# Kernel tuning notes

Hardware: AMD Instinct MI355X
Metric: run time of the kernel (lower is better)

## Reference

```python
import jax, jax.numpy as jnp
import numpy as np

B, T, D, H = 4, 2048, 1024, 16
HD = D // H  # 64
LOCAL_CTX, BLOCKSIZE, VERTSIZE = 256, 1, 16
STRIDE = LOCAL_CTX // BLOCKSIZE  # 256


def build_fixed_mask(n):
    # num_verts == 1 branch of generate_fixed_attention_mask
    layout = np.zeros((n, n), dtype=np.bool_)
    # vertical stripes: top `vertsize` indices of each stride block
    for idx in range(STRIDE - VERTSIZE, STRIDE):
        layout[:, idx::STRIDE] = True
    rows = np.arange(n)
    # local: each query attends to its own stride-block
    same_block = (rows[:, None] // STRIDE) == (rows[None, :] // STRIDE)
    layout |= same_block
    # causal: zero out k > q
    layout &= rows[None, :] <= rows[:, None]
    return layout


def setup_inputs() -> dict:
    key = jax.random.key(0)
    k1, k2, k3, k4, k5 = jax.random.split(key, 5)
    s = 0.02
    return {
        "x": jax.random.normal(k1, (B, T, D), dtype=jnp.float32),
        "Wqkv": jax.random.normal(k2, (D, 3 * D), dtype=jnp.float32) * s,
        "bqkv": jax.random.normal(k3, (3 * D,), dtype=jnp.float32) * s,
        "Wproj": jax.random.normal(k4, (D, D), dtype=jnp.float32) * s,
        "bproj": jax.random.normal(k5, (D,), dtype=jnp.float32) * s,
        "mask": jnp.asarray(build_fixed_mask(T)),
    }


def reference(x, Wqkv, bqkv, Wproj, bproj, mask):
    b, t, _ = x.shape
    qkv = (x @ Wqkv + bqkv).reshape(b, t, 3, H, HD)
    # (B,T,3,H,HD) -> (B,H,T,HD) per component
    q = qkv[:, :, 0].transpose(0, 2, 1, 3)
    k = qkv[:, :, 1].transpose(0, 2, 1, 3)
    v = qkv[:, :, 2].transpose(0, 2, 1, 3)
    att = jnp.einsum("bhqd,bhkd->bhqk", q, k) * (1.0 / jnp.sqrt(jnp.float32(HD)))
    att = jnp.where(mask[:t, :t], att, -jnp.inf)
    att = jax.nn.softmax(att, axis=-1)
    y = jnp.einsum("bhqk,bhkd->bhqd", att, v)
    y = y.transpose(0, 2, 1, 3).reshape(b, t, D)
    return y @ Wproj + bproj
```

## Files before the change

kernel.cpp:

```cpp
#include <hip/hip_runtime.h>
#include <cstdint>
#include <cstddef>

typedef unsigned short u16;
typedef __attribute__((ext_vector_type(8))) short short8;
typedef __attribute__((ext_vector_type(4))) float f32x4;
typedef __attribute__((ext_vector_type(4))) unsigned short u16x4;

#define B_ 4
#define T_ 2048
#define D_ 1024
#define H_ 16
#define HD_ 64

__device__ __forceinline__ u16 f2bf(float f) {
  union { float f; unsigned i; } v; v.f = f;
  unsigned r = (v.i + 0x7FFFu + ((v.i >> 16) & 1u)) >> 16;
  return (u16)r;
}

__device__ __forceinline__ void load_lds16(const void* g, void* l) {
  __builtin_amdgcn_global_load_lds(
      (const __attribute__((address_space(1))) void*)g,
      (__attribute__((address_space(3))) void*)l, 16, 0, 0);
}

__global__ __launch_bounds__(256) void cvt_f32_bf16(const float* __restrict__ src,
                                                    u16* __restrict__ dst) {
  const size_t i = ((size_t)blockIdx.x * 256 + threadIdx.x) * 4;
  const f32x4 v = *(const f32x4*)(src + i);
  u16x4 o;
#pragma unroll
  for (int r = 0; r < 4; ++r) o[r] = f2bf(v[r]);
  *(u16x4*)(dst + i) = o;
}

__global__ __launch_bounds__(256) void transpose_cvt(const float* __restrict__ src,
                                                     u16* __restrict__ dst,
                                                     int R, int C) {
  __shared__ u16 t[32][33];
  const int c0 = blockIdx.x * 32, r0 = blockIdx.y * 32;
  const int tid = threadIdx.x;
  const int lr = tid >> 5, lc = tid & 31;
#pragma unroll
  for (int p = 0; p < 4; ++p)
    t[lr + p * 8][lc] = f2bf(src[(size_t)(r0 + lr + p * 8) * C + c0 + lc]);
  __syncthreads();
#pragma unroll
  for (int p = 0; p < 4; ++p)
    dst[(size_t)(c0 + lr + p * 8) * R + r0 + lc] = t[lc][lr + p * 8];
}

template <int EPI>
__global__ __launch_bounds__(256)
void gemm_bt(const u16* __restrict__ A, const u16* __restrict__ Bt,
             const float* __restrict__ bias, int K, int N,
             void* __restrict__ o0v, u16* __restrict__ o1, u16* __restrict__ o2) {
  __shared__ u16 As[128 * 32];
  __shared__ u16 Bs[128 * 32];
  const int tid = threadIdx.x;
  const int lane = tid & 63;
  const int w = tid >> 6;
  const int q = lane >> 4, col = lane & 15;
  const int m0 = blockIdx.y * 128, n0 = blockIdx.x * 128;
  const int wm = (w >> 1) * 64, wn = (w & 1) * 64;
  const int srow = tid >> 2, soff = (tid & 3) * 8;

  f32x4 acc[4][4] = {};

  const u16* Ap = A + (size_t)(m0 + srow) * K + soff;
  const u16* Bp = Bt + (size_t)(n0 + srow) * K + soff;

  for (int kb = 0; kb < K; kb += 32) {
    load_lds16(Ap + kb, &As[tid * 8]);
    load_lds16(Ap + (size_t)64 * K + kb, &As[2048 + tid * 8]);
    load_lds16(Bp + kb, &Bs[tid * 8]);
    load_lds16(Bp + (size_t)64 * K + kb, &Bs[2048 + tid * 8]);
    __syncthreads();
    short8 af[4], bfr[4];
#pragma unroll
    for (int i = 0; i < 4; ++i)
      af[i] = *(const short8*)&As[(wm + i * 16 + col) * 32 + q * 8];
#pragma unroll
    for (int j = 0; j < 4; ++j)
      bfr[j] = *(const short8*)&Bs[(wn + j * 16 + col) * 32 + q * 8];
#pragma unroll
    for (int i = 0; i < 4; ++i)
#pragma unroll
      for (int j = 0; j < 4; ++j)
        acc[i][j] = __builtin_amdgcn_mfma_f32_16x16x32_bf16(af[i], bfr[j], acc[i][j], 0, 0, 0);
    __syncthreads();
  }

#pragma unroll
  for (int j = 0; j < 4; ++j) {
    const int n = n0 + wn + j * 16 + col;
    const float bv = bias[n];
    if constexpr (EPI == 0) {
      u16* q0p = (u16*)o0v;
      const int c = n >> 10, rem = n & 1023, hh = rem >> 6, dd = rem & 63;
#pragma unroll
      for (int i = 0; i < 4; ++i) {
        const int mrow = m0 + wm + i * 16 + q * 4;
        const int b = mrow >> 11, t = mrow & 2047;
        const int bh = b * H_ + hh;
        if (c == 0) {
#pragma unroll
          for (int r = 0; r < 4; ++r)
            q0p[((size_t)bh * T_ + t + r) * HD_ + dd] = f2bf((acc[i][j][r] + bv) * 0.125f);
        } else if (c == 1) {
#pragma unroll
          for (int r = 0; r < 4; ++r)
            o1[((size_t)bh * T_ + t + r) * HD_ + dd] = f2bf(acc[i][j][r] + bv);
        } else {
          u16x4 pk;
#pragma unroll
          for (int r = 0; r < 4; ++r) pk[r] = f2bf(acc[i][j][r] + bv);
          *(u16x4*)&o2[((size_t)bh * HD_ + dd) * T_ + t] = pk;
        }
      }
    } else {
      float* outp = (float*)o0v;
#pragma unroll
      for (int i = 0; i < 4; ++i) {
        const int mrow = m0 + wm + i * 16 + q * 4;
#pragma unroll
        for (int r = 0; r < 4; ++r)
          outp[(size_t)(mrow + r) * N + n] = acc[i][j][r] + bv;
      }
    }
  }
}

__global__ __launch_bounds__(256)
void sparse_attn(const u16* __restrict__ Qb, const u16* __restrict__ Kb,
                 const u16* __restrict__ Vt, u16* __restrict__ Y) {
  __shared__ char smem[20480];
  u16* Pall = (u16*)smem;
  float* Obuf = (float*)smem;

  const int tid = threadIdx.x, lane = tid & 63, w = tid >> 6;
  const int q = lane >> 4, col = lane & 15;
  const int bh = blockIdx.y, qt = blockIdx.x;
  const int b = bh >> 4, hh = bh & 15;
  const int qb = qt >> 2;
  const int rb = (qt & 3) * 64;
  const int qg = qt * 64;
  const u16* Qh = Qb + (size_t)bh * T_ * HD_;
  const u16* Kh = Kb + (size_t)bh * T_ * HD_;
  const u16* Vh = Vt + (size_t)bh * HD_ * T_;

  short8 qf[4][2];
#pragma unroll
  for (int i = 0; i < 4; ++i)
#pragma unroll
    for (int h2 = 0; h2 < 2; ++h2)
      qf[i][h2] = *(const short8*)&Qh[(size_t)(qg + i * 16 + col) * HD_ + h2 * 32 + q * 8];

  f32x4 o[4][4] = {};
  f32x4 lI[4] = {};
  const short8 ones = {0x3F80, 0x3F80, 0x3F80, 0x3F80, 0x3F80, 0x3F80, 0x3F80, 0x3F80};

  u16* P = Pall + w * 2560;

  const int ns = (qb + 1) >> 1;
  const int L = ns + 2 * (qt & 3) + 2;

  for (int j = w; j < L; j += 4) {
    int k0, k1, localc;
    bool mask1;
    if (j < ns) {
      k0 = (2 * j) * 256 + 240; k1 = k0 + 256;
      mask1 = (2 * j + 1 == qb); localc = -1;
    } else {
      const int c = j - ns;
      k0 = qb * 256 + c * 32; k1 = k0 + 16;
      mask1 = false; localc = c * 32;
    }
    short8 k0a = *(const short8*)&Kh[(size_t)(k0 + col) * HD_ + q * 8];
    short8 k0b = *(const short8*)&Kh[(size_t)(k0 + col) * HD_ + 32 + q * 8];
    short8 k1a = *(const short8*)&Kh[(size_t)(k1 + col) * HD_ + q * 8];
    short8 k1b = *(const short8*)&Kh[(size_t)(k1 + col) * HD_ + 32 + q * 8];
#pragma unroll
    for (int rt = 0; rt < 4; ++rt) {
      f32x4 z = {0.f, 0.f, 0.f, 0.f};
      f32x4 s0 = __builtin_amdgcn_mfma_f32_16x16x32_bf16(qf[rt][0], k0a, z, 0, 0, 0);
      s0 = __builtin_amdgcn_mfma_f32_16x16x32_bf16(qf[rt][1], k0b, s0, 0, 0, 0);
      f32x4 s1 = __builtin_amdgcn_mfma_f32_16x16x32_bf16(qf[rt][0], k1a, z, 0, 0, 0);
      s1 = __builtin_amdgcn_mfma_f32_16x16x32_bf16(qf[rt][1], k1b, s1, 0, 0, 0);
#pragma unroll
      for (int r = 0; r < 4; ++r) {
        float p0 = __expf(s0[r]);
        float p1 = mask1 ? 0.f : __expf(s1[r]);
        if (localc >= 0) {
          const int qr = rb + rt * 16 + q * 4 + r;
          if (localc + col > qr) p0 = 0.f;
          if (localc + 16 + col > qr) p1 = 0.f;
        }
        P[(rt * 16 + q * 4 + r) * 40 + col] = f2bf(p0);
        P[(rt * 16 + q * 4 + r) * 40 + 16 + col] = f2bf(p1);
      }
    }
    asm volatile("s_waitcnt lgkmcnt(0)" ::: "memory");
    short8 pf[4], vf[4];
#pragma unroll
    for (int rt = 0; rt < 4; ++rt)
      pf[rt] = *(const short8*)&P[(rt * 16 + col) * 40 + q * 8];
    const int kvb = (q < 2) ? (k0 + q * 8) : (k1 + (q - 2) * 8);
#pragma unroll
    for (int dt = 0; dt < 4; ++dt)
      vf[dt] = *(const short8*)&Vh[(size_t)(dt * 16 + col) * T_ + kvb];
#pragma unroll
    for (int rt = 0; rt < 4; ++rt) {
#pragma unroll
      for (int dt = 0; dt < 4; ++dt)
        o[rt][dt] = __builtin_amdgcn_mfma_f32_16x16x32_bf16(pf[rt], vf[dt], o[rt][dt], 0, 0, 0);
      lI[rt] = __builtin_amdgcn_mfma_f32_16x16x32_bf16(pf[rt], ones, lI[rt], 0, 0, 0);
    }
  }

#pragma unroll
  for (int rt = 0; rt < 4; ++rt) {
    __syncthreads();
#pragma unroll
    for (int dt = 0; dt < 4; ++dt)
      *(f32x4*)&Obuf[(w * 65 + dt * 16 + col) * 16 + q * 4] = o[rt][dt];
    if (col == 0)
      *(f32x4*)&Obuf[(w * 65 + 64) * 16 + q * 4] = lI[rt];
    __syncthreads();
    f32x4 acc = {0.f, 0.f, 0.f, 0.f};
    f32x4 lt = {0.f, 0.f, 0.f, 0.f};
#pragma unroll
    for (int w2 = 0; w2 < 4; ++w2) {
      acc += *(const f32x4*)&Obuf[(w2 * 65 + w * 16 + col) * 16 + q * 4];
      lt += *(const f32x4*)&Obuf[(w2 * 65 + 64) * 16 + q * 4];
    }
#pragma unroll
    for (int r = 0; r < 4; ++r) {
      const int trow = qg + rt * 16 + q * 4 + r;
      Y[((size_t)(b * T_ + trow)) * D_ + hh * HD_ + w * 16 + col] = f2bf(acc[r] / lt[r]);
    }
  }
}

extern "C" void kernel_launch(void* const* d_in, const int* in_sizes, int n_in,
                              void* d_out, int out_size, void* d_ws, size_t ws_size,
                              hipStream_t stream) {
  const float* x = (const float*)d_in[0];
  const float* Wqkv = (const float*)d_in[1];
  const float* bqkv = (const float*)d_in[2];
  const float* Wproj = (const float*)d_in[3];
  const float* bproj = (const float*)d_in[4];
  float* out = (float*)d_out;

  char* ws = (char*)d_ws;
  u16* xb     = (u16*)(ws + 0);
  u16* WqkvT  = (u16*)(ws + 16777216);
  u16* WprojT = (u16*)(ws + 23068672);
  u16* Qb     = (u16*)(ws + 25165824);
  u16* Kb     = (u16*)(ws + 41943040);
  u16* Vt     = (u16*)(ws + 58720256);
  u16* Y      = (u16*)(ws + 75497472);

  cvt_f32_bf16<<<dim3(8192), 256, 0, stream>>>(x, xb);
  transpose_cvt<<<dim3(96, 32), 256, 0, stream>>>(Wqkv, WqkvT, 1024, 3072);
  transpose_cvt<<<dim3(32, 32), 256, 0, stream>>>(Wproj, WprojT, 1024, 1024);
  gemm_bt<0><<<dim3(24, 64), 256, 0, stream>>>(xb, WqkvT, bqkv, 1024, 3072, Qb, Kb, Vt);
  sparse_attn<<<dim3(32, 64), 256, 0, stream>>>(Qb, Kb, Vt, Y);
  gemm_bt<1><<<dim3(8, 64), 256, 0, stream>>>(Y, WprojT, bproj, 1024, 1024, out, nullptr, nullptr);
}
```

Baseline: 271.7 us.

## Double-buffer GEMMs with swizzled LDS, fuse pre kernels, prefetch K/V in attention

Merges the bf16 conversion and the two weight transposes into one launch. Rewrites the GEMM with double-buffered async LDS loads, an XOR swizzle against bank conflicts, and a block remap meant to spread work across XCDs. The attention loop now prefetches the next K tile and issues the V loads early, and the grid axes are swapped to change scheduling order. The cost is higher register and LDS use.

```diff
diff --git a/kernel.cpp b/kernel.cpp
--- a/kernel.cpp
+++ b/kernel.cpp
@@ -25,22 +25,34 @@
       (__attribute__((address_space(3))) void*)l, 16, 0, 0);
 }
 
-__global__ __launch_bounds__(256) void cvt_f32_bf16(const float* __restrict__ src,
-                                                    u16* __restrict__ dst) {
-  const size_t i = ((size_t)blockIdx.x * 256 + threadIdx.x) * 4;
-  const f32x4 v = *(const f32x4*)(src + i);
-  u16x4 o;
-#pragma unroll
-  for (int r = 0; r < 4; ++r) o[r] = f2bf(v[r]);
-  *(u16x4*)(dst + i) = o;
-}
-
-__global__ __launch_bounds__(256) void transpose_cvt(const float* __restrict__ src,
-                                                     u16* __restrict__ dst,
-                                                     int R, int C) {
+#define RBAR() asm volatile("s_barrier" ::: "memory")
+#define VMC(n) asm volatile("s_waitcnt vmcnt(" #n ")" ::: "memory")
+
+__global__ __launch_bounds__(256)
+void pre_all(const float* __restrict__ x, u16* __restrict__ xb,
+             const float* __restrict__ Wqkv, u16* __restrict__ WqkvT,
+             const float* __restrict__ Wproj, u16* __restrict__ WprojT) {
   __shared__ u16 t[32][33];
-  const int c0 = blockIdx.x * 32, r0 = blockIdx.y * 32;
+  const int bid = blockIdx.x;
   const int tid = threadIdx.x;
+  if (bid < 8192) {
+    const size_t i = ((size_t)bid * 256 + tid) * 4;
+    const f32x4 v = *(const f32x4*)(x + i);
+    u16x4 o;
+#pragma unroll
+    for (int r = 0; r < 4; ++r) o[r] = f2bf(v[r]);
+    *(u16x4*)(xb + i) = o;
+    return;
+  }
+  const float* src; u16* dst; int R, C, bx, by;
+  if (bid < 11264) {
+    const int tb = bid - 8192;
+    bx = tb % 96; by = tb / 96; src = Wqkv; dst = WqkvT; R = 1024; C = 3072;
+  } else {
+    const int tb = bid - 11264;
+    bx = tb & 31; by = tb >> 5; src = Wproj; dst = WprojT; R = 1024; C = 1024;
+  }
+  const int c0 = bx * 32, r0 = by * 32;
   const int lr = tid >> 5, lc = tid & 31;
 #pragma unroll
   for (int p = 0; p < 4; ++p)
@@ -53,43 +65,65 @@
 
 template <int EPI>
 __global__ __launch_bounds__(256)
-void gemm_bt(const u16* __restrict__ A, const u16* __restrict__ Bt,
+void gemm_db(const u16* __restrict__ A, const u16* __restrict__ Bt,
              const float* __restrict__ bias, int K, int N,
              void* __restrict__ o0v, u16* __restrict__ o1, u16* __restrict__ o2) {
-  __shared__ u16 As[128 * 32];
-  __shared__ u16 Bs[128 * 32];
+  __shared__ u16 As[2][4096];
+  __shared__ u16 Bs[2][4096];
   const int tid = threadIdx.x;
   const int lane = tid & 63;
   const int w = tid >> 6;
   const int q = lane >> 4, col = lane & 15;
-  const int m0 = blockIdx.y * 128, n0 = blockIdx.x * 128;
+
+  const int nbx = gridDim.x;
+  const int id = blockIdx.y * nbx + blockIdx.x;
+  const int nwg = nbx * gridDim.y;
+  const int sid = (id & 7) * (nwg >> 3) + (id >> 3);
+  const int m0 = (sid / nbx) * 128, n0 = (sid % nbx) * 128;
+
   const int wm = (w >> 1) * 64, wn = (w & 1) * 64;
-  const int srow = tid >> 2, soff = (tid & 3) * 8;
+
+  const int srow = tid >> 2;
+  const int cb8 = ((tid & 3) ^ ((tid >> 3) & 3)) << 3;
+  const u16* Ap = A + (size_t)(m0 + srow) * K + cb8;
+  const u16* Bp = Bt + (size_t)(n0 + srow) * K + cb8;
+
+  const int rs = (q ^ ((col >> 1) & 3)) << 3;
 
   f32x4 acc[4][4] = {};
 
-  const u16* Ap = A + (size_t)(m0 + srow) * K + soff;
-  const u16* Bp = Bt + (size_t)(n0 + srow) * K + soff;
-
-  for (int kb = 0; kb < K; kb += 32) {
-    load_lds16(Ap + kb, &As[tid * 8]);
-    load_lds16(Ap + (size_t)64 * K + kb, &As[2048 + tid * 8]);
-    load_lds16(Bp + kb, &Bs[tid * 8]);
-    load_lds16(Bp + (size_t)64 * K + kb, &Bs[2048 + tid * 8]);
-    __syncthreads();
+  auto STAGE = [&](int b, int kb) {
+    load_lds16(Ap + kb, &As[b][tid * 8]);
+    load_lds16(Ap + (size_t)64 * K + kb, &As[b][2048 + tid * 8]);
+    load_lds16(Bp + kb, &Bs[b][tid * 8]);
+    load_lds16(Bp + (size_t)64 * K + kb, &Bs[b][2048 + tid * 8]);
+  };
+
+  const int NT = K >> 5;
+  STAGE(0, 0);
+
+  for (int t = 0; t < NT; ++t) {
+    const int b = t & 1;
+    if (t + 1 < NT) {
+      STAGE(b ^ 1, (t + 1) << 5);
+      VMC(4);
+    } else {
+      VMC(0);
+    }
+    RBAR();
     short8 af[4], bfr[4];
 #pragma unroll
     for (int i = 0; i < 4; ++i)
-      af[i] = *(const short8*)&As[(wm + i * 16 + col) * 32 + q * 8];
+      af[i] = *(const short8*)&As[b][(wm + i * 16 + col) * 32 + rs];
 #pragma unroll
     for (int j = 0; j < 4; ++j)
-      bfr[j] = *(const short8*)&Bs[(wn + j * 16 + col) * 32 + q * 8];
+      bfr[j] = *(const short8*)&Bs[b][(wn + j * 16 + col) * 32 + rs];
 #pragma unroll
     for (int i = 0; i < 4; ++i)
 #pragma unroll
       for (int j = 0; j < 4; ++j)
         acc[i][j] = __builtin_amdgcn_mfma_f32_16x16x32_bf16(af[i], bfr[j], acc[i][j], 0, 0, 0);
-    __syncthreads();
+    RBAR();
   }
 
 #pragma unroll
@@ -141,7 +175,7 @@
 
   const int tid = threadIdx.x, lane = tid & 63, w = tid >> 6;
   const int q = lane >> 4, col = lane & 15;
-  const int bh = blockIdx.y, qt = blockIdx.x;
+  const int bh = blockIdx.x, qt = blockIdx.y;
   const int b = bh >> 4, hh = bh & 15;
   const int qb = qt >> 2;
   const int rb = (qt & 3) * 64;
@@ -166,9 +200,7 @@
   const int ns = (qb + 1) >> 1;
   const int L = ns + 2 * (qt & 3) + 2;
 
-  for (int j = w; j < L; j += 4) {
-    int k0, k1, localc;
-    bool mask1;
+  auto params = [&](int j, int& k0, int& k1, bool& mask1, int& localc) {
     if (j < ns) {
       k0 = (2 * j) * 256 + 240; k1 = k0 + 256;
       mask1 = (2 * j + 1 == qb); localc = -1;
@@ -177,17 +209,38 @@
       k0 = qb * 256 + c * 32; k1 = k0 + 16;
       mask1 = false; localc = c * 32;
     }
-    short8 k0a = *(const short8*)&Kh[(size_t)(k0 + col) * HD_ + q * 8];
-    short8 k0b = *(const short8*)&Kh[(size_t)(k0 + col) * HD_ + 32 + q * 8];
-    short8 k1a = *(const short8*)&Kh[(size_t)(k1 + col) * HD_ + q * 8];
-    short8 k1b = *(const short8*)&Kh[(size_t)(k1 + col) * HD_ + 32 + q * 8];
+  };
+  auto ldK = [&](int k0, int k1, short8* kf) {
+    kf[0] = *(const short8*)&Kh[(size_t)(k0 + col) * HD_ + q * 8];
+    kf[1] = *(const short8*)&Kh[(size_t)(k0 + col) * HD_ + 32 + q * 8];
+    kf[2] = *(const short8*)&Kh[(size_t)(k1 + col) * HD_ + q * 8];
+    kf[3] = *(const short8*)&Kh[(size_t)(k1 + col) * HD_ + 32 + q * 8];
+  };
+
+  int k0 = 0, k1 = 0, localc = -1;
+  bool mask1 = false;
+  short8 kf[4];
+  if (w < L) { params(w, k0, k1, mask1, localc); ldK(k0, k1, kf); }
+
+  for (int j = w; j < L; j += 4) {
+    const int kvb = (q < 2) ? (k0 + q * 8) : (k1 + (q - 2) * 8);
+    short8 vf[4];
+#pragma unroll
+    for (int dt = 0; dt < 4; ++dt)
+      vf[dt] = *(const short8*)&Vh[(size_t)(dt * 16 + col) * T_ + kvb];
+    int nk0 = 0, nk1 = 0, nlocalc = -1;
+    bool nmask1 = false;
+    short8 nkf[4];
+    const bool hn = (j + 4) < L;
+    if (hn) { params(j + 4, nk0, nk1, nmask1, nlocalc); ldK(nk0, nk1, nkf); }
+
 #pragma unroll
     for (int rt = 0; rt < 4; ++rt) {
       f32x4 z = {0.f, 0.f, 0.f, 0.f};
-      f32x4 s0 = __builtin_amdgcn_mfma_f32_16x16x32_bf16(qf[rt][0], k0a, z, 0, 0, 0);
-      s0 = __builtin_amdgcn_mfma_f32_16x16x32_bf16(qf[rt][1], k0b, s0, 0, 0, 0);
-      f32x4 s1 = __builtin_amdgcn_mfma_f32_16x16x32_bf16(qf[rt][0], k1a, z, 0, 0, 0);
-      s1 = __builtin_amdgcn_mfma_f32_16x16x32_bf16(qf[rt][1], k1b, s1, 0, 0, 0);
+      f32x4 s0 = __builtin_amdgcn_mfma_f32_16x16x32_bf16(qf[rt][0], kf[0], z, 0, 0, 0);
+      s0 = __builtin_amdgcn_mfma_f32_16x16x32_bf16(qf[rt][1], kf[1], s0, 0, 0, 0);
+      f32x4 s1 = __builtin_amdgcn_mfma_f32_16x16x32_bf16(qf[rt][0], kf[2], z, 0, 0, 0);
+      s1 = __builtin_amdgcn_mfma_f32_16x16x32_bf16(qf[rt][1], kf[3], s1, 0, 0, 0);
 #pragma unroll
       for (int r = 0; r < 4; ++r) {
         float p0 = __expf(s0[r]);
@@ -202,20 +255,20 @@
       }
     }
     asm volatile("s_waitcnt lgkmcnt(0)" ::: "memory");
-    short8 pf[4], vf[4];
+    short8 pf[4];
 #pragma unroll
     for (int rt = 0; rt < 4; ++rt)
       pf[rt] = *(const short8*)&P[(rt * 16 + col) * 40 + q * 8];
-    const int kvb = (q < 2) ? (k0 + q * 8) : (k1 + (q - 2) * 8);
-#pragma unroll
-    for (int dt = 0; dt < 4; ++dt)
-      vf[dt] = *(const short8*)&Vh[(size_t)(dt * 16 + col) * T_ + kvb];
 #pragma unroll
     for (int rt = 0; rt < 4; ++rt) {
 #pragma unroll
       for (int dt = 0; dt < 4; ++dt)
         o[rt][dt] = __builtin_amdgcn_mfma_f32_16x16x32_bf16(pf[rt], vf[dt], o[rt][dt], 0, 0, 0);
       lI[rt] = __builtin_amdgcn_mfma_f32_16x16x32_bf16(pf[rt], ones, lI[rt], 0, 0, 0);
+    }
+    if (hn) {
+      k0 = nk0; k1 = nk1; mask1 = nmask1; localc = nlocalc;
+      kf[0] = nkf[0]; kf[1] = nkf[1]; kf[2] = nkf[2]; kf[3] = nkf[3];
     }
   }
 
@@ -262,10 +315,8 @@
   u16* Vt     = (u16*)(ws + 58720256);
   u16* Y      = (u16*)(ws + 75497472);
 
-  cvt_f32_bf16<<<dim3(8192), 256, 0, stream>>>(x, xb);
-  transpose_cvt<<<dim3(96, 32), 256, 0, stream>>>(Wqkv, WqkvT, 1024, 3072);
-  transpose_cvt<<<dim3(32, 32), 256, 0, stream>>>(Wproj, WprojT, 1024, 1024);
-  gemm_bt<0><<<dim3(24, 64), 256, 0, stream>>>(xb, WqkvT, bqkv, 1024, 3072, Qb, Kb, Vt);
-  sparse_attn<<<dim3(32, 64), 256, 0, stream>>>(Qb, Kb, Vt, Y);
-  gemm_bt<1><<<dim3(8, 64), 256, 0, stream>>>(Y, WprojT, bproj, 1024, 1024, out, nullptr, nullptr);
-}
+  pre_all<<<dim3(12288), 256, 0, stream>>>(x, xb, Wqkv, WqkvT, Wproj, WprojT);
+  gemm_db<0><<<dim3(24, 64), 256, 0, stream>>>(xb, WqkvT, bqkv, 1024, 3072, Qb, Kb, Vt);
+  sparse_attn<<<dim3(64, 32), 256, 0, stream>>>(Qb, Kb, Vt, Y);
+  gemm_db<1><<<dim3(8, 64), 256, 0, stream>>>(Y, WprojT, bproj, 1024, 1024, out, nullptr, nullptr);
+}
```

After: 241.2 us. -11.2%, faster.
